# Kernel optimization log

Hardware: AMD Instinct MI355X
Metric: run time of the kernel (lower is better)

The kernel has to match this reference:

```python
import jax, jax.numpy as jnp
import numpy as np
import math

N_EMBD = 1024
HEADS = 16
DIM_HEAD = 64
INNER = HEADS * DIM_HEAD
VIS_DIM = 768
PROMPT_DIM = 768
SCALE = DIM_HEAD ** -0.5


def layer_norm(x, w, b, eps=1e-5):
    mu = jnp.mean(x, axis=-1, keepdims=True)
    var = jnp.var(x, axis=-1, keepdims=True)
    return (x - mu) * jax.lax.rsqrt(var + eps) * w + b


def new_gelu(x):
    c = math.sqrt(2.0 / math.pi)
    return 0.5 * x * (1.0 + jnp.tanh(c * (x + 0.044715 * x ** 3)))


def cross_attn(x, ctx, wq, wk, wv, wo, bo):
    # x: [B,T,Dq], ctx: [B,S,Dc]; weights stored [in,out]
    B, T, _ = x.shape
    S = ctx.shape[1]
    q = (x @ wq).reshape(B, T, HEADS, DIM_HEAD).transpose(0, 2, 1, 3)
    k = (ctx @ wk).reshape(B, S, HEADS, DIM_HEAD).transpose(0, 2, 1, 3)
    v = (ctx @ wv).reshape(B, S, HEADS, DIM_HEAD).transpose(0, 2, 1, 3)
    sim = jnp.einsum('bhid,bhjd->bhij', q, k) * SCALE  # [B,H,T,S]
    attn = jax.nn.softmax(sim, axis=-1)
    out = jnp.einsum('bhij,bhjd->bhid', attn, v)
    out = out.transpose(0, 2, 1, 3).reshape(B, T, INNER)
    return out @ wo + bo


def setup_inputs() -> dict:
    key = jax.random.key(0)
    ks = jax.random.split(key, 24)
    s = 0.02
    d = {
        'x': jax.random.normal(ks[0], (256, 60, N_EMBD), jnp.float32),
        'img_embd': jax.random.normal(ks[1], (256, 197, VIS_DIM), jnp.float32),
        'prompt_embd': jax.random.normal(ks[2], (256, 77, PROMPT_DIM), jnp.float32),
        'ln1_w': jnp.ones(N_EMBD), 'ln1_b': jnp.zeros(N_EMBD),
        'ln2_w': jnp.ones(N_EMBD), 'ln2_b': jnp.zeros(N_EMBD),
        'ln3_w': jnp.ones(N_EMBD), 'ln3_b': jnp.zeros(N_EMBD),
        'ln4_w': jnp.ones(N_EMBD), 'ln4_b': jnp.zeros(N_EMBD),
        'sa_wq': jax.random.normal(ks[3], (N_EMBD, INNER)) * s,
        'sa_wk': jax.random.normal(ks[4], (N_EMBD, INNER)) * s,
        'sa_wv': jax.random.normal(ks[5], (N_EMBD, INNER)) * s,
        'sa_wo': jax.random.normal(ks[6], (INNER, N_EMBD)) * s,
        'sa_bo': jnp.zeros(N_EMBD),
        'ia_wq': jax.random.normal(ks[7], (N_EMBD, INNER)) * s,
        'ia_wk': jax.random.normal(ks[8], (VIS_DIM, INNER)) * s,
        'ia_wv': jax.random.normal(ks[9], (VIS_DIM, INNER)) * s,
        'ia_wo': jax.random.normal(ks[10], (INNER, N_EMBD)) * s,
        'ia_bo': jnp.zeros(N_EMBD),
        'pa_wq': jax.random.normal(ks[11], (N_EMBD, INNER)) * s,
        'pa_wk': jax.random.normal(ks[12], (PROMPT_DIM, INNER)) * s,
        'pa_wv': jax.random.normal(ks[13], (PROMPT_DIM, INNER)) * s,
        'pa_wo': jax.random.normal(ks[14], (INNER, N_EMBD)) * s,
        'pa_bo': jnp.zeros(N_EMBD),
        'fc_w': jax.random.normal(ks[15], (N_EMBD, 4 * N_EMBD)) * s,
        'fc_b': jnp.zeros(4 * N_EMBD),
        'proj_w': jax.random.normal(ks[16], (4 * N_EMBD, N_EMBD)) * s,
        'proj_b': jnp.zeros(N_EMBD),
    }
    return d


def reference(x, img_embd, prompt_embd,
              ln1_w, ln1_b, ln2_w, ln2_b, ln3_w, ln3_b, ln4_w, ln4_b,
              sa_wq, sa_wk, sa_wv, sa_wo, sa_bo,
              ia_wq, ia_wk, ia_wv, ia_wo, ia_bo,
              pa_wq, pa_wk, pa_wv, pa_wo, pa_bo,
              fc_w, fc_b, proj_w, proj_b):
    h = layer_norm(x, ln1_w, ln1_b)
    x = x + cross_attn(h, h, sa_wq, sa_wk, sa_wv, sa_wo, sa_bo)
    x = x + cross_attn(layer_norm(x, ln2_w, ln2_b), img_embd, ia_wq, ia_wk, ia_wv, ia_wo, ia_bo)
    x = x + cross_attn(layer_norm(x, ln3_w, ln3_b), prompt_embd, pa_wq, pa_wk, pa_wv, pa_wo, pa_bo)
    h = layer_norm(x, ln4_w, ln4_b)
    x = x + (new_gelu(h @ fc_w + fc_b) @ proj_w + proj_b)
    return x
```

## Files before the change

kernel.cpp:

```cpp
#include <hip/hip_runtime.h>

typedef __bf16 bf16;
typedef __bf16 bf16x8 __attribute__((ext_vector_type(8)));
typedef float  f32x4  __attribute__((ext_vector_type(4)));

#define N_EMBD 1024
#define HEADS 16
#define DIM_HEAD 64


__device__ __forceinline__ void async_load16(const bf16* g, bf16* l) {
    __builtin_amdgcn_global_load_lds(
        (const __attribute__((address_space(1))) void*)g,
        (__attribute__((address_space(3))) void*)l, 16, 0, 0);
}

__device__ __forceinline__ float gelu_f(float x) {
    const float c = 0.7978845608028654f;
    float u = c * (x + 0.044715f * x * x * x);
    return 0.5f * x * (1.0f + tanhf(u));
}


__global__ __launch_bounds__(256) void cvt_f32_bf16(const float* __restrict__ in,
                                                    bf16* __restrict__ out, int n) {
    int i = (blockIdx.x * 256 + threadIdx.x) * 8;
    if (i >= n) return;
    bf16x8 v;
    #pragma unroll
    for (int j = 0; j < 8; j++) v[j] = (bf16)in[i + j];
    *(bf16x8*)&out[i] = v;
}


__global__ __launch_bounds__(256) void transpose_k(const float* __restrict__ in,
                                                   bf16* __restrict__ out, int R, int C) {
    __shared__ bf16 tile[32][33];
    int c0 = blockIdx.x * 32, r0 = blockIdx.y * 32;
    int tx = threadIdx.x, ty = threadIdx.y;
    #pragma unroll
    for (int j = 0; j < 4; j++)
        tile[ty + j * 8][tx] = (bf16)in[(size_t)(r0 + ty + j * 8) * C + c0 + tx];
    __syncthreads();
    #pragma unroll
    for (int j = 0; j < 4; j++)
        out[(size_t)(c0 + ty + j * 8) * R + r0 + tx] = tile[tx][ty + j * 8];
}


__global__ __launch_bounds__(256) void ln_kernel(const float* __restrict__ x,
                                                 const float* __restrict__ w,
                                                 const float* __restrict__ b,
                                                 bf16* __restrict__ out) {
    int row = blockIdx.x;
    int tid = threadIdx.x;
    const float* xr = x + (size_t)row * N_EMBD;
    float4 v = *(const float4*)&xr[tid * 4];
    float s  = v.x + v.y + v.z + v.w;
    float s2 = v.x * v.x + v.y * v.y + v.z * v.z + v.w * v.w;
    #pragma unroll
    for (int off = 32; off >= 1; off >>= 1) {
        s  += __shfl_down(s, off);
        s2 += __shfl_down(s2, off);
    }
    __shared__ float red[8];
    int wave = tid >> 6, lane = tid & 63;
    if (lane == 0) { red[wave] = s; red[4 + wave] = s2; }
    __syncthreads();
    s  = red[0] + red[1] + red[2] + red[3];
    s2 = red[4] + red[5] + red[6] + red[7];
    float mu  = s * (1.0f / N_EMBD);
    float var = s2 * (1.0f / N_EMBD) - mu * mu;
    float r = 1.0f / sqrtf(var + 1e-5f);
    bf16* orow = out + (size_t)row * N_EMBD;
    float vv[4] = {v.x, v.y, v.z, v.w};
    #pragma unroll
    for (int j = 0; j < 4; j++) {
        int c = tid * 4 + j;
        float y = (vv[j] - mu) * r * w[c] + b[c];
        orow[c] = (bf16)y;
    }
}


__global__ __launch_bounds__(256) void gemm_bt(
    const bf16* __restrict__ A, const bf16* __restrict__ B,
    bf16* __restrict__ Cout, float* __restrict__ Cacc,
    const float* __restrict__ bias,
    int M, int N, int K, int ldc, int act)
{
    __shared__ __align__(16) bf16 As[128][64];
    __shared__ __align__(16) bf16 Bs[128][64];
    const int tid  = threadIdx.x;
    const int wave = tid >> 6, lane = tid & 63;
    const int waveRow = (wave & 1) * 64, waveCol = (wave >> 1) * 64;
    const int blockN = blockIdx.x * 128, blockM = blockIdx.y * 128;

    f32x4 acc[4][4];
    #pragma unroll
    for (int r = 0; r < 4; r++)
        #pragma unroll
        for (int c = 0; c < 4; c++) acc[r][c] = (f32x4)0.0f;

    const int lr = lane >> 3;
    const int lc = (lane & 7) * 8;
    const size_t arow = (size_t)(blockM + wave * 32 + lr) * K;
    const size_t brow = (size_t)(blockN + wave * 32 + lr) * K;

    for (int k0 = 0; k0 < K; k0 += 64) {
        __syncthreads();
        #pragma unroll
        for (int i = 0; i < 4; i++) {
            async_load16(A + arow + (size_t)i * 8 * K + k0 + lc, &As[wave * 32 + i * 8][0]);
            async_load16(B + brow + (size_t)i * 8 * K + k0 + lc, &Bs[wave * 32 + i * 8][0]);
        }
        __syncthreads();
        #pragma unroll
        for (int ks = 0; ks < 2; ks++) {
            bf16x8 af[4], bq[4];
            #pragma unroll
            for (int r = 0; r < 4; r++)
                af[r] = *(const bf16x8*)&As[waveRow + r * 16 + (lane & 15)][ks * 32 + (lane >> 4) * 8];
            #pragma unroll
            for (int c = 0; c < 4; c++)
                bq[c] = *(const bf16x8*)&Bs[waveCol + c * 16 + (lane & 15)][ks * 32 + (lane >> 4) * 8];
            #pragma unroll
            for (int r = 0; r < 4; r++)
                #pragma unroll
                for (int c = 0; c < 4; c++)
                    acc[r][c] = __builtin_amdgcn_mfma_f32_16x16x32_bf16(af[r], bq[c], acc[r][c], 0, 0, 0);
        }
    }

    const int row0 = blockM + waveRow + ((lane >> 4) << 2);
    const int col0 = blockN + waveCol + (lane & 15);
    #pragma unroll
    for (int r = 0; r < 4; r++) {
        #pragma unroll
        for (int c = 0; c < 4; c++) {
            int cc = col0 + c * 16;
            float bv = bias ? bias[cc] : 0.0f;
            #pragma unroll
            for (int j = 0; j < 4; j++) {
                int row = row0 + r * 16 + j;
                float v = acc[r][c][j] + bv;
                if (act) v = gelu_f(v);
                if (Cacc) Cacc[(size_t)row * ldc + cc] += v;
                else      Cout[(size_t)row * ldc + cc] = (bf16)v;
            }
        }
    }
}


__global__ __launch_bounds__(256) void attn_mfma(
    const bf16* __restrict__ Q, int ldq,
    const bf16* __restrict__ K, const bf16* __restrict__ V, int ldkv,
    bf16* __restrict__ O, int ldo,
    int T, int S, float scale)
{
    const int b = blockIdx.x >> 4, h = blockIdx.x & 15;
    const int tid = threadIdx.x;
    const int wave = tid >> 6, lane = tid & 63;
    const int l15 = lane & 15, g = lane >> 4;

    __shared__ __align__(16) bf16 Ks[64][72];
    __shared__ __align__(16) bf16 Vt[64][72];
    __shared__ __align__(16) bf16 Ps[64][72];

    const int qm = wave * 16 + l15;
    const bf16* qrow = Q + (size_t)(b * T + (qm < T ? qm : 0)) * ldq + h * DIM_HEAD;
    bf16x8 aq[2];
    #pragma unroll
    for (int kk = 0; kk < 2; kk++) {
        bf16x8 t = *(const bf16x8*)&qrow[kk * 32 + g * 8];
        #pragma unroll
        for (int j = 0; j < 8; j++) t[j] = (bf16)((float)t[j] * scale);
        aq[kk] = t;
    }

    float m_run[4], l_run[4];
    f32x4 acc_o[4];
    #pragma unroll
    for (int r = 0; r < 4; r++) { m_run[r] = -1e30f; l_run[r] = 0.0f; acc_o[r] = (f32x4)0.0f; }

    for (int s0 = 0; s0 < S; s0 += 64) {
        __syncthreads();
        for (int i = tid; i < 512; i += 256) {
            int r = i >> 3, c = (i & 7) * 8;
            int s = s0 + r;
            if (s < S) {
                size_t gidx = (size_t)(b * S + s) * ldkv + h * DIM_HEAD + c;
                *(int4*)&Ks[r][c] = *(const int4*)&K[gidx];
                bf16x8 v = *(const bf16x8*)&V[gidx];
                #pragma unroll
                for (int j = 0; j < 8; j++) Vt[c + j][r] = v[j];
            } else {
                int4 z; z.x = z.y = z.z = z.w = 0;
                *(int4*)&Ks[r][c] = z;
                #pragma unroll
                for (int j = 0; j < 8; j++) Vt[c + j][r] = (bf16)0.0f;
            }
        }
        __syncthreads();

        f32x4 sc[4];
        #pragma unroll
        for (int jn = 0; jn < 4; jn++) {
            f32x4 s = (f32x4)0.0f;
            bf16x8 bk0 = *(const bf16x8*)&Ks[jn * 16 + l15][g * 8];
            bf16x8 bk1 = *(const bf16x8*)&Ks[jn * 16 + l15][32 + g * 8];
            s = __builtin_amdgcn_mfma_f32_16x16x32_bf16(aq[0], bk0, s, 0, 0, 0);
            s = __builtin_amdgcn_mfma_f32_16x16x32_bf16(aq[1], bk1, s, 0, 0, 0);
            sc[jn] = s;
        }
        #pragma unroll
        for (int jn = 0; jn < 4; jn++)
            if (s0 + jn * 16 + l15 >= S) sc[jn] = (f32x4)(-1e30f);

        float mx[4];
        #pragma unroll
        for (int r = 0; r < 4; r++)
            mx[r] = fmaxf(fmaxf(sc[0][r], sc[1][r]), fmaxf(sc[2][r], sc[3][r]));
        #pragma unroll
        for (int off = 1; off < 16; off <<= 1)
            #pragma unroll
            for (int r = 0; r < 4; r++) mx[r] = fmaxf(mx[r], __shfl_xor(mx[r], off));
        float al[4];
        #pragma unroll
        for (int r = 0; r < 4; r++) {
            float mn = fmaxf(m_run[r], mx[r]);
            al[r] = __expf(m_run[r] - mn);
            m_run[r] = mn;
        }
        float rs[4] = {0.f, 0.f, 0.f, 0.f};
        #pragma unroll
        for (int jn = 0; jn < 4; jn++)
            #pragma unroll
            for (int r = 0; r < 4; r++) {
                float p = __expf(sc[jn][r] - m_run[r]);
                sc[jn][r] = p;
                rs[r] += p;
            }
        #pragma unroll
        for (int off = 1; off < 16; off <<= 1)
            #pragma unroll
            for (int r = 0; r < 4; r++) rs[r] += __shfl_xor(rs[r], off);
        #pragma unroll
        for (int r = 0; r < 4; r++) l_run[r] = l_run[r] * al[r] + rs[r];
        #pragma unroll
        for (int jd = 0; jd < 4; jd++)
            #pragma unroll
            for (int r = 0; r < 4; r++) acc_o[jd][r] *= al[r];

        #pragma unroll
        for (int jn = 0; jn < 4; jn++)
            #pragma unroll
            for (int r = 0; r < 4; r++)
                Ps[wave * 16 + g * 4 + r][jn * 16 + l15] = (bf16)sc[jn][r];
        __syncthreads();

        #pragma unroll
        for (int kk = 0; kk < 2; kk++) {
            bf16x8 ap = *(const bf16x8*)&Ps[wave * 16 + l15][kk * 32 + g * 8];
            #pragma unroll
            for (int jd = 0; jd < 4; jd++) {
                bf16x8 bv = *(const bf16x8*)&Vt[jd * 16 + l15][kk * 32 + g * 8];
                acc_o[jd] = __builtin_amdgcn_mfma_f32_16x16x32_bf16(ap, bv, acc_o[jd], 0, 0, 0);
            }
        }
    }

    #pragma unroll
    for (int r = 0; r < 4; r++) {
        int q = wave * 16 + g * 4 + r;
        if (q < T) {
            float inv = 1.0f / l_run[r];
            bf16* orow = O + (size_t)(b * T + q) * ldo + h * DIM_HEAD;
            #pragma unroll
            for (int jd = 0; jd < 4; jd++)
                orow[jd * 16 + l15] = (bf16)(acc_o[jd][r] * inv);
        }
    }
}


extern "C" void kernel_launch(void* const* d_in, const int* in_sizes, int n_in,
                              void* d_out, int out_size, void* d_ws, size_t ws_size,
                              hipStream_t stream) {
    const int B = 256, T = 60, S_IMG = 197, S_PR = 77;
    const int MQ = B * T;
    const int M_PR = B * S_PR;
    const float scale = 0.125f;

    const float* x_in   = (const float*)d_in[0];
    const float* img    = (const float*)d_in[1];
    const float* prompt = (const float*)d_in[2];
    const float* ln1w = (const float*)d_in[3],  *ln1b = (const float*)d_in[4];
    const float* ln2w = (const float*)d_in[5],  *ln2b = (const float*)d_in[6];
    const float* ln3w = (const float*)d_in[7],  *ln3b = (const float*)d_in[8];
    const float* ln4w = (const float*)d_in[9],  *ln4b = (const float*)d_in[10];
    const float* sa_bo = (const float*)d_in[15];
    const float* ia_bo = (const float*)d_in[20];
    const float* pa_bo = (const float*)d_in[25];
    const float* fc_b  = (const float*)d_in[27];
    const float* pj_b  = (const float*)d_in[29];

    char* ws = (char*)d_ws;
    float* x_f32 = (float*)ws;
    bf16*  h     = (bf16*)(ws + 62914560);
    bf16*  ao    = h;
    bf16*  qkv   = (bf16*)(ws + 94371840);
    bf16*  Rkv   = (bf16*)(ws + 188743680);
    bf16*  Rcv   = (bf16*)(ws + 188743680 + 103284736);
    bf16*  wT    = (bf16*)(ws + 330760192);
    bf16*  hidden = Rkv;

    struct TJ { int idx; size_t off; int R, C; };
    const TJ jobs[14] = {
        {11, 0,        1024, 1024},
        {12, 1048576,  1024, 1024},
        {13, 2097152,  1024, 1024},
        {14, 3145728,  1024, 1024},
        {16, 4194304,  1024, 1024},
        {17, 5242880,  768,  1024},
        {18, 6029312,  768,  1024},
        {19, 6815744,  1024, 1024},
        {21, 7864320,  1024, 1024},
        {22, 8912896,  768,  1024},
        {23, 9699328,  768,  1024},
        {24, 10485760, 1024, 1024},
        {26, 11534336, 1024, 4096},
        {28, 15728640, 4096, 1024},
    };
    for (int i = 0; i < 14; i++) {
        dim3 g(jobs[i].C / 32, jobs[i].R / 32), blk(32, 8);
        transpose_k<<<g, blk, 0, stream>>>((const float*)d_in[jobs[i].idx], wT + jobs[i].off,
                                           jobs[i].R, jobs[i].C);
    }

    hipMemcpyAsync(x_f32, x_in, (size_t)MQ * N_EMBD * 4, hipMemcpyDeviceToDevice, stream);

    auto gemm = [&](const bf16* A, const bf16* Bw, bf16* Co, float* Ca, const float* bias,
                    int M, int N, int K, int ldc, int act) {
        gemm_bt<<<dim3(N / 128, M / 128), 256, 0, stream>>>(A, Bw, Co, Ca, bias, M, N, K, ldc, act);
    };

    ln_kernel<<<MQ, 256, 0, stream>>>(x_f32, ln1w, ln1b, h);
    gemm(h, wT + 0, qkv, nullptr, nullptr, MQ, 3072, 1024, 3072, 0);
    attn_mfma<<<B * HEADS, 256, 0, stream>>>(qkv, 3072, qkv + 1024, qkv + 2048, 3072,
                                             ao, 1024, T, T, scale);
    gemm(ao, wT + 3145728, nullptr, x_f32, sa_bo, MQ, 1024, 1024, 1024, 0);

    ln_kernel<<<MQ, 256, 0, stream>>>(x_f32, ln2w, ln2b, h);
    gemm(h, wT + 4194304, qkv, nullptr, nullptr, MQ, 1024, 1024, 1024, 0);
    {
        const int BC = 128, Mc = BC * S_IMG;
        for (int c = 0; c < 2; c++) {
            const float* imgc = img + (size_t)c * Mc * 768;
            cvt_f32_bf16<<<(Mc * 768) / 2048, 256, 0, stream>>>(imgc, Rcv, Mc * 768);
            gemm(Rcv, wT + 5242880, Rkv, nullptr, nullptr, Mc, 2048, 768, 2048, 0);
            attn_mfma<<<BC * HEADS, 256, 0, stream>>>(
                qkv + (size_t)c * BC * T * 1024, 1024, Rkv, Rkv + 1024, 2048,
                ao + (size_t)c * BC * T * 1024, 1024, T, S_IMG, scale);
        }
    }
    gemm(ao, wT + 6815744, nullptr, x_f32, ia_bo, MQ, 1024, 1024, 1024, 0);

    ln_kernel<<<MQ, 256, 0, stream>>>(x_f32, ln3w, ln3b, h);
    gemm(h, wT + 7864320, qkv, nullptr, nullptr, MQ, 1024, 1024, 1024, 0);
    cvt_f32_bf16<<<(M_PR * 768) / 2048, 256, 0, stream>>>(prompt, Rcv, M_PR * 768);
    gemm(Rcv, wT + 8912896, Rkv, nullptr, nullptr, M_PR, 2048, 768, 2048, 0);
    attn_mfma<<<B * HEADS, 256, 0, stream>>>(qkv, 1024, Rkv, Rkv + 1024, 2048,
                                             ao, 1024, T, S_PR, scale);
    gemm(ao, wT + 10485760, nullptr, x_f32, pa_bo, MQ, 1024, 1024, 1024, 0);

    ln_kernel<<<MQ, 256, 0, stream>>>(x_f32, ln4w, ln4b, h);
    gemm(h, wT + 11534336, hidden, nullptr, fc_b, MQ, 4096, 1024, 4096, 1);
    gemm(hidden, wT + 15728640, nullptr, x_f32, pj_b, MQ, 1024, 4096, 1024, 0);

    hipMemcpyAsync(d_out, x_f32, (size_t)MQ * N_EMBD * 4, hipMemcpyDeviceToDevice, stream);
}
```

Measured before the change: 2.233 ms.

## Replace GEMM with 256x256 double-buffered swizzled-LDS kernel and XCD-aware tile mapping

```diff
diff --git a/kernel.cpp b/kernel.cpp
--- a/kernel.cpp
+++ b/kernel.cpp
@@ -83,70 +83,177 @@
 }
 
 
-__global__ __launch_bounds__(256) void gemm_bt(
+__global__ __launch_bounds__(512, 2) void gemm_bt256(
     const bf16* __restrict__ A, const bf16* __restrict__ B,
     bf16* __restrict__ Cout, float* __restrict__ Cacc,
     const float* __restrict__ bias,
-    int M, int N, int K, int ldc, int act)
+    int M, int N, int K, int ldc, int act, int gn)
 {
-    __shared__ __align__(16) bf16 As[128][64];
-    __shared__ __align__(16) bf16 Bs[128][64];
-    const int tid  = threadIdx.x;
-    const int wave = tid >> 6, lane = tid & 63;
-    const int waveRow = (wave & 1) * 64, waveCol = (wave >> 1) * 64;
-    const int blockN = blockIdx.x * 128, blockM = blockIdx.y * 128;
-
-    f32x4 acc[4][4];
-    #pragma unroll
-    for (int r = 0; r < 4; r++)
-        #pragma unroll
-        for (int c = 0; c < 4; c++) acc[r][c] = (f32x4)0.0f;
-
-    const int lr = lane >> 3;
-    const int lc = (lane & 7) * 8;
-    const size_t arow = (size_t)(blockM + wave * 32 + lr) * K;
-    const size_t brow = (size_t)(blockN + wave * 32 + lr) * K;
-
-    for (int k0 = 0; k0 < K; k0 += 64) {
-        __syncthreads();
-        #pragma unroll
-        for (int i = 0; i < 4; i++) {
-            async_load16(A + arow + (size_t)i * 8 * K + k0 + lc, &As[wave * 32 + i * 8][0]);
-            async_load16(B + brow + (size_t)i * 8 * K + k0 + lc, &Bs[wave * 32 + i * 8][0]);
-        }
-        __syncthreads();
-        #pragma unroll
-        for (int ks = 0; ks < 2; ks++) {
-            bf16x8 af[4], bq[4];
-            #pragma unroll
-            for (int r = 0; r < 4; r++)
-                af[r] = *(const bf16x8*)&As[waveRow + r * 16 + (lane & 15)][ks * 32 + (lane >> 4) * 8];
-            #pragma unroll
-            for (int c = 0; c < 4; c++)
-                bq[c] = *(const bf16x8*)&Bs[waveCol + c * 16 + (lane & 15)][ks * 32 + (lane >> 4) * 8];
-            #pragma unroll
-            for (int r = 0; r < 4; r++)
-                #pragma unroll
-                for (int c = 0; c < 4; c++)
-                    acc[r][c] = __builtin_amdgcn_mfma_f32_16x16x32_bf16(af[r], bq[c], acc[r][c], 0, 0, 0);
-        }
-    }
-
-    const int row0 = blockM + waveRow + ((lane >> 4) << 2);
-    const int col0 = blockN + waveCol + (lane & 15);
-    #pragma unroll
-    for (int r = 0; r < 4; r++) {
-        #pragma unroll
-        for (int c = 0; c < 4; c++) {
-            int cc = col0 + c * 16;
+    extern __shared__ __align__(16) bf16 smem[];
+    bf16 (*As)[256][64] = (bf16(*)[256][64])smem;
+    bf16 (*Bs)[256][64] = (bf16(*)[256][64])(smem + 2 * 256 * 64);
+
+    const int tid = threadIdx.x;
+    const int wv = tid >> 6, lane = tid & 63;
+    const int l15 = lane & 15, g = lane >> 4;
+    const int waveM = wv >> 2, waveN = wv & 3;
+
+    const int nwg = gridDim.x;
+    const int bid = blockIdx.x;
+    const int q = nwg >> 3, r8 = nwg & 7;
+    const int xcd = bid & 7, idx = bid >> 3;
+    const int swz = (xcd < r8 ? xcd * (q + 1) : r8 * (q + 1) + (xcd - r8) * q) + idx;
+    const int tileM = (swz / gn) * 256;
+    const int tileN = (swz % gn) * 256;
+
+    const int NT = K >> 6;
+
+    f32x4 acc[8][4];
+    #pragma unroll
+    for (int i = 0; i < 8; i++)
+        #pragma unroll
+        for (int j = 0; j < 4; j++) acc[i][j] = (f32x4)0.0f;
+
+    const int rr = tid >> 3;
+    const int kc0 = tid & 7;
+
+    auto stage = [&](int t2) {
+        const int nb = t2 & 1;
+        const int k0 = t2 << 6;
+        #pragma unroll
+        for (int j = 0; j < 4; ++j) {
+            int row = j * 64 + rr;
+            int kc = kc0 ^ (row & 7);
+            int ar = tileM + row; if (ar >= M) ar = M - 1;
+            async_load16(A + (size_t)ar * K + k0 + kc * 8,
+                         &As[nb][0][0] + ((size_t)j * 512 + wv * 64) * 8);
+        }
+        #pragma unroll
+        for (int j = 0; j < 4; ++j) {
+            int row = j * 64 + rr;
+            int kc = kc0 ^ (row & 7);
+            async_load16(B + (size_t)(tileN + row) * K + k0 + kc * 8,
+                         &Bs[nb][0][0] + ((size_t)j * 512 + wv * 64) * 8);
+        }
+    };
+
+    stage(0);
+
+    for (int t = 0; t < NT; ++t) {
+        const int cur = t & 1;
+        __builtin_amdgcn_sched_barrier(0);
+        if (t + 1 < NT) {
+            stage(t + 1);
+            __builtin_amdgcn_sched_barrier(0);
+            asm volatile("s_waitcnt vmcnt(8)" ::: "memory");
+        } else {
+            __builtin_amdgcn_sched_barrier(0);
+            asm volatile("s_waitcnt vmcnt(0)" ::: "memory");
+        }
+        __builtin_amdgcn_sched_barrier(0);
+        __builtin_amdgcn_s_barrier();
+        __builtin_amdgcn_sched_barrier(0);
+
+        bf16x8 a[4][2], b0[2][2], b1[2][2];
+
+        #pragma unroll
+        for (int mf = 0; mf < 4; ++mf)
+            #pragma unroll
+            for (int ks = 0; ks < 2; ++ks) {
+                int r2 = waveM * 128 + mf * 16 + l15;
+                a[mf][ks] = *(const bf16x8*)&As[cur][r2][(((ks << 2) + g) ^ (l15 & 7)) << 3];
+            }
+        #pragma unroll
+        for (int nf = 0; nf < 2; ++nf)
+            #pragma unroll
+            for (int ks = 0; ks < 2; ++ks) {
+                int r2 = waveN * 64 + nf * 16 + l15;
+                b0[nf][ks] = *(const bf16x8*)&Bs[cur][r2][(((ks << 2) + g) ^ (l15 & 7)) << 3];
+            }
+        __builtin_amdgcn_s_setprio(1);
+        #pragma unroll
+        for (int mf = 0; mf < 4; ++mf)
+            #pragma unroll
+            for (int nf = 0; nf < 2; ++nf)
+                #pragma unroll
+                for (int ks = 0; ks < 2; ++ks)
+                    acc[mf][nf] = __builtin_amdgcn_mfma_f32_16x16x32_bf16(a[mf][ks], b0[nf][ks], acc[mf][nf], 0, 0, 0);
+        __builtin_amdgcn_s_setprio(0);
+        __builtin_amdgcn_sched_barrier(0);
+        __builtin_amdgcn_s_barrier();
+        __builtin_amdgcn_sched_barrier(0);
+
+        #pragma unroll
+        for (int nf = 0; nf < 2; ++nf)
+            #pragma unroll
+            for (int ks = 0; ks < 2; ++ks) {
+                int r2 = waveN * 64 + (2 + nf) * 16 + l15;
+                b1[nf][ks] = *(const bf16x8*)&Bs[cur][r2][(((ks << 2) + g) ^ (l15 & 7)) << 3];
+            }
+        __builtin_amdgcn_s_setprio(1);
+        #pragma unroll
+        for (int mf = 0; mf < 4; ++mf)
+            #pragma unroll
+            for (int nf = 0; nf < 2; ++nf)
+                #pragma unroll
+                for (int ks = 0; ks < 2; ++ks)
+                    acc[mf][2 + nf] = __builtin_amdgcn_mfma_f32_16x16x32_bf16(a[mf][ks], b1[nf][ks], acc[mf][2 + nf], 0, 0, 0);
+        __builtin_amdgcn_s_setprio(0);
+        __builtin_amdgcn_sched_barrier(0);
+        __builtin_amdgcn_s_barrier();
+        __builtin_amdgcn_sched_barrier(0);
+
+        #pragma unroll
+        for (int mf = 0; mf < 4; ++mf)
+            #pragma unroll
+            for (int ks = 0; ks < 2; ++ks) {
+                int r2 = waveM * 128 + 64 + mf * 16 + l15;
+                a[mf][ks] = *(const bf16x8*)&As[cur][r2][(((ks << 2) + g) ^ (l15 & 7)) << 3];
+            }
+        __builtin_amdgcn_s_setprio(1);
+        #pragma unroll
+        for (int mf = 0; mf < 4; ++mf)
+            #pragma unroll
+            for (int nf = 0; nf < 2; ++nf)
+                #pragma unroll
+                for (int ks = 0; ks < 2; ++ks)
+                    acc[4 + mf][2 + nf] = __builtin_amdgcn_mfma_f32_16x16x32_bf16(a[mf][ks], b1[nf][ks], acc[4 + mf][2 + nf], 0, 0, 0);
+        __builtin_amdgcn_s_setprio(0);
+        __builtin_amdgcn_sched_barrier(0);
+        __builtin_amdgcn_s_barrier();
+        __builtin_amdgcn_sched_barrier(0);
+
+        __builtin_amdgcn_s_setprio(1);
+        #pragma unroll
+        for (int mf = 0; mf < 4; ++mf)
+            #pragma unroll
+            for (int nf = 0; nf < 2; ++nf)
+                #pragma unroll
+                for (int ks = 0; ks < 2; ++ks)
+                    acc[4 + mf][nf] = __builtin_amdgcn_mfma_f32_16x16x32_bf16(a[mf][ks], b0[nf][ks], acc[4 + mf][nf], 0, 0, 0);
+        __builtin_amdgcn_s_setprio(0);
+        __builtin_amdgcn_sched_barrier(0);
+        __builtin_amdgcn_s_barrier();
+        __builtin_amdgcn_sched_barrier(0);
+    }
+
+    const int row0 = tileM + waveM * 128 + (g << 2);
+    const int col0 = tileN + waveN * 64 + l15;
+    #pragma unroll
+    for (int mf = 0; mf < 8; ++mf) {
+        #pragma unroll
+        for (int nf = 0; nf < 4; ++nf) {
+            int cc = col0 + nf * 16;
             float bv = bias ? bias[cc] : 0.0f;
             #pragma unroll
-            for (int j = 0; j < 4; j++) {
-                int row = row0 + r * 16 + j;
-                float v = acc[r][c][j] + bv;
-                if (act) v = gelu_f(v);
-                if (Cacc) Cacc[(size_t)row * ldc + cc] += v;
-                else      Cout[(size_t)row * ldc + cc] = (bf16)v;
+            for (int j = 0; j < 4; ++j) {
+                int rw = row0 + mf * 16 + j;
+                if (rw < M) {
+                    float v = acc[mf][nf][j] + bv;
+                    if (act) v = gelu_f(v);
+                    if (Cacc) Cacc[(size_t)rw * ldc + cc] += v;
+                    else      Cout[(size_t)rw * ldc + cc] = (bf16)v;
+                }
             }
         }
     }
@@ -273,10 +380,10 @@
 
     #pragma unroll
     for (int r = 0; r < 4; r++) {
-        int q = wave * 16 + g * 4 + r;
-        if (q < T) {
+        int qq = wave * 16 + g * 4 + r;
+        if (qq < T) {
             float inv = 1.0f / l_run[r];
-            bf16* orow = O + (size_t)(b * T + q) * ldo + h * DIM_HEAD;
+            bf16* orow = O + (size_t)(b * T + qq) * ldo + h * DIM_HEAD;
             #pragma unroll
             for (int jd = 0; jd < 4; jd++)
                 orow[jd * 16 + l15] = (bf16)(acc_o[jd][r] * inv);
@@ -341,9 +448,10 @@
 
     hipMemcpyAsync(x_f32, x_in, (size_t)MQ * N_EMBD * 4, hipMemcpyDeviceToDevice, stream);
 
-    auto gemm = [&](const bf16* A, const bf16* Bw, bf16* Co, float* Ca, const float* bias,
+    auto gemm = [&](const bf16* Aa, const bf16* Bw, bf16* Co, float* Ca, const float* bias,
                     int M, int N, int K, int ldc, int act) {
-        gemm_bt<<<dim3(N / 128, M / 128), 256, 0, stream>>>(A, Bw, Co, Ca, bias, M, N, K, ldc, act);
+        int gm = (M + 255) / 256, gn = N / 256;
+        gemm_bt256<<<gm * gn, 512, 131072, stream>>>(Aa, Bw, Co, Ca, bias, M, N, K, ldc, act, gn);
     };
 
     ln_kernel<<<MQ, 256, 0, stream>>>(x_f32, ln1w, ln1b, h);
```

Result: faster. 2.105 ms (-5.7%).
